# Optimization experiments

Hardware: AMD Instinct MI355X
Metric: run time of the kernel (lower is better)

Reference implementation:

```python
import jax, jax.numpy as jnp
import numpy as np

WS = 7          # window_size
HEADS = 6
HEAD_DIM = 32
DISP = WS // 2  # displacement = 3
NEG = -1e9      # stands in for -inf in shift masks (safe for grads/low precision)


def _rel_indices():
    # get_relative_distances(window_size) + window_size - 1
    pos = np.array([[i, j] for i in range(WS) for j in range(WS)])  # (49, 2)
    return pos[None, :, :] - pos[:, None, :] + WS - 1               # (49, 49, 2)


def _shift_mask(nw_h, nw_w):
    # per-window additive mask replicating upper_lower_mask / left_right_mask placement
    n = WS * WS
    ul = np.zeros((n, n), np.float32)
    ul[-DISP * WS:, :-DISP * WS] = NEG
    ul[:-DISP * WS, -DISP * WS:] = NEG
    m4 = np.zeros((WS, WS, WS, WS), np.float32)
    m4[:, -DISP:, :, :-DISP] = NEG
    m4[:, :-DISP, :, -DISP:] = NEG
    lr = m4.reshape(n, n)
    full = np.zeros((nw_h, nw_w, n, n), np.float32)
    full[-1, :] += ul              # dots[:, :, -nw_w:] += upper_lower_mask
    full[:, -1] += lr              # dots[:, :, nw_w-1::nw_w] += left_right_mask
    return full.reshape(nw_h * nw_w, n, n)


def setup_inputs() -> dict:
    key = jax.random.key(0)
    k1, k2, k3, k4 = jax.random.split(key, 4)
    dim, inner = 192, HEADS * HEAD_DIM
    return {
        "x": jax.random.normal(k1, (16, 56, 56, dim), jnp.float32),
        "w_qkv": jax.random.normal(k2, (dim, inner * 3), jnp.float32) * 0.02,
        "pos_embedding": jax.random.normal(k3, (2 * WS - 1, 2 * WS - 1), jnp.float32),
        "w_out": jax.random.normal(k4, (inner, dim), jnp.float32) * 0.02,
        "b_out": jnp.zeros((dim,), jnp.float32),
    }


def reference(x, w_qkv, pos_embedding, w_out, b_out):
    b, H, W, dim = x.shape
    nw_h, nw_w = H // WS, W // WS
    x = jnp.roll(x, (-DISP, -DISP), axis=(1, 2))          # shifted window
    qkv = x @ w_qkv                                       # [b,H,W,3*inner]
    q, k, v = jnp.split(qkv, 3, axis=-1)

    def to_windows(t):  # [b,H,W,inner] -> [b,h,nw,ws*ws,d]
        t = t.reshape(b, nw_h, WS, nw_w, WS, HEADS, HEAD_DIM)
        return t.transpose(0, 5, 1, 3, 2, 4, 6).reshape(b, HEADS, nw_h * nw_w, WS * WS, HEAD_DIM)

    q, k, v = to_windows(q), to_windows(k), to_windows(v)
    scale = HEAD_DIM ** -0.5
    dots = jnp.einsum('bhwid,bhwjd->bhwij', q, k) * scale  # [b,h,nw,49,49]

    rel = _rel_indices()
    bias = pos_embedding[rel[..., 0], rel[..., 1]]         # [49,49]
    dots = dots + bias
    dots = dots + jnp.asarray(_shift_mask(nw_h, nw_w))     # broadcast over b,h

    attn = jax.nn.softmax(dots, axis=-1)
    out = jnp.einsum('bhwij,bhwjd->bhwid', attn, v)        # [b,h,nw,49,d]
    out = out.reshape(b, HEADS, nw_h, nw_w, WS, WS, HEAD_DIM)
    out = out.transpose(0, 2, 4, 3, 5, 1, 6).reshape(b, H, W, HEADS * HEAD_DIM)
    out = out @ w_out + b_out
    return jnp.roll(out, (DISP, DISP), axis=(1, 2))
```

## Files before the change

### kernel.cpp

```cpp
#include <hip/hip_runtime.h>
#include <hip/hip_bf16.h>

typedef __bf16 bf16_t;
typedef __bf16 bf16x8 __attribute__((ext_vector_type(8)));
typedef float f32x4 __attribute__((ext_vector_type(4)));
typedef unsigned int u32;

#define NB 16
#define HW 56
#define DIM 192
#define N3 576
#define WS7 7
#define HEADS 6
#define HD 32
#define NTOK 49
#define MFMA(a, b, c) __builtin_amdgcn_mfma_f32_16x16x32_bf16(a, b, c, 0, 0, 0)

__device__ __forceinline__ void gld_lds16(const bf16_t* g, bf16_t* l) {
    __builtin_amdgcn_global_load_lds((const __attribute__((address_space(1))) u32*)g,
                                     (__attribute__((address_space(3))) u32*)l, 16, 0, 0);
}

__global__ __launch_bounds__(256) void prep_x_kernel(const float* __restrict__ x,
                                                     bf16_t* __restrict__ xb) {
    int idx = blockIdx.x * 256 + threadIdx.x;
    const int total = NB * HW * HW * (DIM / 8);
    if (idx >= total) return;
    int c8 = idx % (DIM / 8);
    int p  = idx / (DIM / 8);
    int xx = p % HW;
    int yy = (p / HW) % HW;
    int bb = p / (HW * HW);
    int ys = yy + 3; if (ys >= HW) ys -= HW;
    int xs = xx + 3; if (xs >= HW) xs -= HW;
    const float* src = x + ((size_t)(bb * HW + ys) * HW + xs) * DIM + c8 * 8;
    float4 a0 = *reinterpret_cast<const float4*>(src);
    float4 a1 = *reinterpret_cast<const float4*>(src + 4);
    bf16x8 o;
    o[0] = (bf16_t)a0.x; o[1] = (bf16_t)a0.y; o[2] = (bf16_t)a0.z; o[3] = (bf16_t)a0.w;
    o[4] = (bf16_t)a1.x; o[5] = (bf16_t)a1.y; o[6] = (bf16_t)a1.z; o[7] = (bf16_t)a1.w;
    *reinterpret_cast<bf16x8*>(xb + (size_t)idx * 8) = o;
}

__global__ __launch_bounds__(256) void prep_w_kernel(const float* __restrict__ wqkv,
                                                     const float* __restrict__ wout,
                                                     bf16_t* __restrict__ wqkvt,
                                                     bf16_t* __restrict__ woutt) {
    int idx = blockIdx.x * 256 + threadIdx.x;
    if (idx < N3 * DIM) {
        int k = idx % DIM, n = idx / DIM;
        wqkvt[idx] = (bf16_t)wqkv[(size_t)k * N3 + n];
    } else {
        int j = idx - N3 * DIM;
        if (j < DIM * DIM) {
            int k = j % DIM, n = j / DIM;
            woutt[j] = (bf16_t)wout[(size_t)k * DIM + n];
        }
    }
}

__global__ __launch_bounds__(256) void prep_tbl_kernel(const float* __restrict__ pe,
                                                       float* __restrict__ tbl) {
    int idx = blockIdx.x * 256 + threadIdx.x;
    if (idx >= 4 * 64 * 64) return;
    int v = idx >> 12, rem = idx & 4095, ti = rem >> 6, tj = rem & 63;
    float val = -1e9f;
    if (ti < NTOK && tj < NTOK) {
        int yi = ti / 7, xi = ti % 7, yj = tj / 7, xj = tj % 7;
        val = pe[(yj - yi + 6) * 13 + (xj - xi + 6)];
        bool mr = (v & 2) && ((yi >= 4) != (yj >= 4));
        bool mc = (v & 1) && ((xi >= 4) != (xj >= 4));
        if (mr || mc) val = -1e9f;
    }
    tbl[idx] = val;
}

__global__ __launch_bounds__(256) void qkv_gemm5(const bf16_t* __restrict__ xb,
                                                 const bf16_t* __restrict__ wt,
                                                 bf16_t* __restrict__ qkv) {
    __shared__ alignas(16) bf16_t bsh[64 * DIM];
    const int nblk = blockIdx.y;
    const int wave = threadIdx.x >> 6, lane = threadIdx.x & 63;
    const int lo = lane & 15, hi = lane >> 4;

    const bf16_t* bt = wt + (size_t)nblk * 64 * DIM;
#pragma unroll
    for (int i = 0; i < 6; i++) {
        int s = wave * 384 + i * 64 + lane;
        int g = s ^ ((s / 24) & 7);
        gld_lds16(bt + g * 8, bsh + (wave * 384 + i * 64) * 8);
    }

    const size_t rowbase = (size_t)blockIdx.x * 512 + wave * 32;
    const float qs = (nblk < 3) ? 0.17677669529663687f : 1.0f;

    auto load_tile = [&](bf16x8 (&a)[2][6], int t) {
        const bf16_t* ab = xb + (rowbase + t * 128 + lo) * DIM + hi * 8;
#pragma unroll
        for (int mtl = 0; mtl < 2; mtl++)
#pragma unroll
            for (int ks = 0; ks < 6; ks++)
                a[mtl][ks] = *reinterpret_cast<const bf16x8*>(ab + mtl * 16 * DIM + ks * 32);
    };

    auto compute_store = [&](bf16x8 (&a)[2][6], int t) {
        f32x4 acc[2][4];
#pragma unroll
        for (int mtl = 0; mtl < 2; mtl++)
#pragma unroll
            for (int ct = 0; ct < 4; ct++) acc[mtl][ct] = (f32x4){0.f, 0.f, 0.f, 0.f};
#pragma unroll
        for (int ks = 0; ks < 6; ks++)
#pragma unroll
            for (int ct = 0; ct < 4; ct++) {
                int r = ct * 16 + lo;
                int off = (ks * 64 + hi * 16) ^ ((r & 7) << 4);
                bf16x8 b = *reinterpret_cast<const bf16x8*>((const char*)bsh + r * 384 + off);
#pragma unroll
                for (int mtl = 0; mtl < 2; mtl++)
                    acc[mtl][ct] = MFMA(a[mtl][ks], b, acc[mtl][ct]);
            }
        const size_t rb = rowbase + t * 128;
#pragma unroll
        for (int mtl = 0; mtl < 2; mtl++)
#pragma unroll
            for (int ct = 0; ct < 4; ct++)
#pragma unroll
                for (int r = 0; r < 4; r++)
                    qkv[(rb + mtl * 16 + hi * 4 + r) * N3 + nblk * 64 + ct * 16 + lo] =
                        (bf16_t)(acc[mtl][ct][r] * qs);
    };

    bf16x8 A0[2][6], A1[2][6];
    load_tile(A0, 0);
    __syncthreads();

#pragma unroll
    for (int t = 0; t < 4; t += 2) {
        load_tile(A1, t + 1);
        compute_store(A0, t);
        if (t + 2 < 4) load_tile(A0, t + 2);
        compute_store(A1, t + 1);
    }
}

__global__ __launch_bounds__(256) void attn_kernel4(const bf16_t* __restrict__ qkv,
                                                    const float* __restrict__ tbl,
                                                    bf16_t* __restrict__ att) {
    const int win = blockIdx.x, h = blockIdx.y, bb = blockIdx.z;
    const int wh = win >> 3, ww = win & 7;
    const int mt = threadIdx.x >> 6;
    const int lane = threadIdx.x & 63;
    const int lo = lane & 15, hi = lane >> 4;

    __shared__ bf16_t P[64][72];
    __shared__ alignas(16) bf16_t VT[32][72];

    const int variant = ((wh == 7) ? 2 : 0) | ((ww == 7) ? 1 : 0);
    const float* tbase = tbl + ((size_t)variant << 12);

    auto tokoff = [&](int t) -> size_t {
        int ti = t / 7, tj = t % 7;
        return ((size_t)(bb * HW + wh * WS7 + ti) * HW + ww * WS7 + tj) * N3 + h * HD;
    };

    {
        const int t = mt * 16 + lo;
        bf16x8 v;
        if (t < NTOK) {
            v = *reinterpret_cast<const bf16x8*>(qkv + tokoff(t) + 2 * DIM + hi * 8);
        } else {
#pragma unroll
            for (int j = 0; j < 8; j++) v[j] = (bf16_t)0.f;
        }
#pragma unroll
        for (int j = 0; j < 8; j++) VT[hi * 8 + j][t] = v[j];
    }

    bf16x8 qf, kf[4];
    {
        int t = mt * 16 + lo;
        if (t < NTOK) {
            qf = *reinterpret_cast<const bf16x8*>(qkv + tokoff(t) + hi * 8);
        } else {
#pragma unroll
            for (int j = 0; j < 8; j++) qf[j] = (bf16_t)0.f;
        }
    }
#pragma unroll
    for (int ct = 0; ct < 4; ct++) {
        int t = ct * 16 + lo;
        if (t < NTOK) {
            kf[ct] = *reinterpret_cast<const bf16x8*>(qkv + tokoff(t) + DIM + hi * 8);
        } else {
#pragma unroll
            for (int j = 0; j < 8; j++) kf[ct][j] = (bf16_t)0.f;
        }
    }

    const f32x4 zero4 = {0.f, 0.f, 0.f, 0.f};
    f32x4 s[4];
#pragma unroll
    for (int ct = 0; ct < 4; ct++) s[ct] = MFMA(qf, kf[ct], zero4);

    float rinv[4];
#pragma unroll
    for (int r = 0; r < 4; r++) {
        int ti = mt * 16 + hi * 4 + r;
        const float* trow = tbase + ti * 64 + lo;
        float vals[4];
        float mx = -3e38f;
#pragma unroll
        for (int ct = 0; ct < 4; ct++) {
            float v = s[ct][r] + trow[ct * 16];
            vals[ct] = v;
            mx = fmaxf(mx, v);
        }
#pragma unroll
        for (int off = 1; off < 16; off <<= 1) mx = fmaxf(mx, __shfl_xor(mx, off));
        float sum = 0.f;
#pragma unroll
        for (int ct = 0; ct < 4; ct++) {
            float p = __expf(vals[ct] - mx);
            sum += p;
            P[ti][ct * 16 + lo] = (bf16_t)p;
        }
#pragma unroll
        for (int off = 1; off < 16; off <<= 1) sum += __shfl_xor(sum, off);
        rinv[r] = 1.f / sum;
    }

    __syncthreads();

    f32x4 o[2] = {zero4, zero4};
#pragma unroll
    for (int ks = 0; ks < 2; ks++) {
        bf16x8 pa = *reinterpret_cast<const bf16x8*>(&P[mt * 16 + lo][ks * 32 + hi * 8]);
#pragma unroll
        for (int c2 = 0; c2 < 2; c2++) {
            bf16x8 vb = *reinterpret_cast<const bf16x8*>(&VT[c2 * 16 + lo][ks * 32 + hi * 8]);
            o[c2] = MFMA(pa, vb, o[c2]);
        }
    }

#pragma unroll
    for (int r = 0; r < 4; r++) {
        int ti = mt * 16 + hi * 4 + r;
        if (ti < NTOK) {
            int y = wh * WS7 + ti / 7, xcol = ww * WS7 + ti % 7;
            size_t aoff = ((size_t)(bb * HW + y) * HW + xcol) * DIM + h * HD;
#pragma unroll
            for (int c2 = 0; c2 < 2; c2++)
                att[aoff + c2 * 16 + lo] = (bf16_t)(o[c2][r] * rinv[r]);
        }
    }
}

__global__ __launch_bounds__(256) void out_gemm2(const bf16_t* __restrict__ att,
                                                 const bf16_t* __restrict__ wt,
                                                 const float* __restrict__ bias,
                                                 float* __restrict__ out) {
    __shared__ alignas(16) bf16_t bsh[64 * DIM];
    const int mblk = blockIdx.x, nblk = blockIdx.y;
    const int wave = threadIdx.x >> 6, lane = threadIdx.x & 63;
    const int lo = lane & 15, hi = lane >> 4;

    const bf16_t* bt = wt + (size_t)nblk * 64 * DIM;
#pragma unroll
    for (int i = 0; i < 6; i++) {
        int s = wave * 384 + i * 64 + lane;
        int g = s ^ ((s / 24) & 7);
        gld_lds16(bt + g * 8, bsh + (wave * 384 + i * 64) * 8);
    }

    bf16x8 a[2][6];
    const bf16_t* ab = att + ((size_t)mblk * 128 + wave * 32 + lo) * DIM + hi * 8;
#pragma unroll
    for (int mt = 0; mt < 2; mt++)
#pragma unroll
        for (int ks = 0; ks < 6; ks++)
            a[mt][ks] = *reinterpret_cast<const bf16x8*>(ab + mt * 16 * DIM + ks * 32);

    f32x4 acc[2][4];
#pragma unroll
    for (int mt = 0; mt < 2; mt++)
#pragma unroll
        for (int ct = 0; ct < 4; ct++) acc[mt][ct] = (f32x4){0.f, 0.f, 0.f, 0.f};

    __syncthreads();

#pragma unroll
    for (int ks = 0; ks < 6; ks++)
#pragma unroll
        for (int ct = 0; ct < 4; ct++) {
            int r = ct * 16 + lo;
            int off = (ks * 64 + hi * 16) ^ ((r & 7) << 4);
            bf16x8 b = *reinterpret_cast<const bf16x8*>((const char*)bsh + r * 384 + off);
            acc[0][ct] = MFMA(a[0][ks], b, acc[0][ct]);
            acc[1][ct] = MFMA(a[1][ks], b, acc[1][ct]);
        }

    const int rb = mblk * 128 + wave * 32;
#pragma unroll
    for (int mt = 0; mt < 2; mt++)
#pragma unroll
        for (int r = 0; r < 4; r++) {
            int m = rb + mt * 16 + hi * 4 + r;
            int bb = m / (HW * HW);
            int rem = m - bb * HW * HW;
            int ya = rem / HW, xa = rem - ya * HW;
            int yo = ya + 3; if (yo >= HW) yo -= HW;
            int xo = xa + 3; if (xo >= HW) xo -= HW;
            size_t ob = ((size_t)(bb * HW + yo) * HW + xo) * DIM + nblk * 64;
#pragma unroll
            for (int ct = 0; ct < 4; ct++)
                out[ob + ct * 16 + lo] = acc[mt][ct][r] + bias[nblk * 64 + ct * 16 + lo];
        }
}

extern "C" void kernel_launch(void* const* d_in, const int* in_sizes, int n_in,
                              void* d_out, int out_size, void* d_ws, size_t ws_size,
                              hipStream_t stream) {
    const float* x    = (const float*)d_in[0];
    const float* wqkv = (const float*)d_in[1];
    const float* pe   = (const float*)d_in[2];
    const float* wout = (const float*)d_in[3];
    const float* bout = (const float*)d_in[4];
    float* out = (float*)d_out;

    char* ws = (char*)d_ws;
    const size_t XB_BYTES  = (size_t)NB * HW * HW * DIM * 2;
    const size_t QKV_BYTES = (size_t)NB * HW * HW * N3 * 2;
    const size_t ATT_BYTES = XB_BYTES;
    const size_t WQ_BYTES  = (size_t)N3 * DIM * 2;
    const size_t WO_BYTES  = (size_t)DIM * DIM * 2;
    bf16_t* xb    = (bf16_t*)ws;
    bf16_t* qkv   = (bf16_t*)(ws + XB_BYTES);
    bf16_t* att   = (bf16_t*)(ws + XB_BYTES + QKV_BYTES);
    bf16_t* wqkvt = (bf16_t*)(ws + XB_BYTES + QKV_BYTES + ATT_BYTES);
    bf16_t* woutt = (bf16_t*)(ws + XB_BYTES + QKV_BYTES + ATT_BYTES + WQ_BYTES);
    float*  tbl   = (float*)(ws + XB_BYTES + QKV_BYTES + ATT_BYTES + WQ_BYTES + WO_BYTES);

    prep_x_kernel<<<(NB * HW * HW * (DIM / 8) + 255) / 256, 256, 0, stream>>>(x, xb);
    prep_w_kernel<<<(N3 * DIM + DIM * DIM + 255) / 256, 256, 0, stream>>>(wqkv, wout, wqkvt, woutt);
    prep_tbl_kernel<<<64, 256, 0, stream>>>(pe, tbl);
    qkv_gemm5<<<dim3(98, 9), 256, 0, stream>>>(xb, wqkvt, qkv);
    attn_kernel4<<<dim3(64, HEADS, NB), 256, 0, stream>>>(qkv, tbl, att);
    out_gemm2<<<dim3(392, 3), 256, 0, stream>>>(att, woutt, bout, out);
}
```

Baseline: 176.7 us.

## Fuse QKV projection into window attention kernel, eliminating the qkv buffer

Removes the separate QKV GEMM. Each attention block now loads its window's 49 tokens of x, computes its own head's Q, K and V with MFMA against weights read straight from global memory, and stages them in LDS before the existing softmax and PV steps. This avoids writing and re-reading the large bf16 qkv intermediate. In exchange, x is re-read once per head, weight tiles are fetched through L2 by every block, and each block does more serial work. The grid is reordered so the six heads of a window run adjacently, improving L2 reuse of x.

New measurement: 232.2 us. +31.5%, slower.

```diff
diff --git a/kernel.cpp b/kernel.cpp
--- a/kernel.cpp
+++ b/kernel.cpp
@@ -75,134 +75,73 @@
     tbl[idx] = val;
 }
 
-__global__ __launch_bounds__(256) void qkv_gemm5(const bf16_t* __restrict__ xb,
-                                                 const bf16_t* __restrict__ wt,
-                                                 bf16_t* __restrict__ qkv) {
-    __shared__ alignas(16) bf16_t bsh[64 * DIM];
-    const int nblk = blockIdx.y;
-    const int wave = threadIdx.x >> 6, lane = threadIdx.x & 63;
-    const int lo = lane & 15, hi = lane >> 4;
-
-    const bf16_t* bt = wt + (size_t)nblk * 64 * DIM;
-#pragma unroll
-    for (int i = 0; i < 6; i++) {
-        int s = wave * 384 + i * 64 + lane;
-        int g = s ^ ((s / 24) & 7);
-        gld_lds16(bt + g * 8, bsh + (wave * 384 + i * 64) * 8);
-    }
-
-    const size_t rowbase = (size_t)blockIdx.x * 512 + wave * 32;
-    const float qs = (nblk < 3) ? 0.17677669529663687f : 1.0f;
-
-    auto load_tile = [&](bf16x8 (&a)[2][6], int t) {
-        const bf16_t* ab = xb + (rowbase + t * 128 + lo) * DIM + hi * 8;
-#pragma unroll
-        for (int mtl = 0; mtl < 2; mtl++)
-#pragma unroll
-            for (int ks = 0; ks < 6; ks++)
-                a[mtl][ks] = *reinterpret_cast<const bf16x8*>(ab + mtl * 16 * DIM + ks * 32);
-    };
-
-    auto compute_store = [&](bf16x8 (&a)[2][6], int t) {
-        f32x4 acc[2][4];
-#pragma unroll
-        for (int mtl = 0; mtl < 2; mtl++)
-#pragma unroll
-            for (int ct = 0; ct < 4; ct++) acc[mtl][ct] = (f32x4){0.f, 0.f, 0.f, 0.f};
-#pragma unroll
-        for (int ks = 0; ks < 6; ks++)
-#pragma unroll
-            for (int ct = 0; ct < 4; ct++) {
-                int r = ct * 16 + lo;
-                int off = (ks * 64 + hi * 16) ^ ((r & 7) << 4);
-                bf16x8 b = *reinterpret_cast<const bf16x8*>((const char*)bsh + r * 384 + off);
-#pragma unroll
-                for (int mtl = 0; mtl < 2; mtl++)
-                    acc[mtl][ct] = MFMA(a[mtl][ks], b, acc[mtl][ct]);
-            }
-        const size_t rb = rowbase + t * 128;
-#pragma unroll
-        for (int mtl = 0; mtl < 2; mtl++)
-#pragma unroll
-            for (int ct = 0; ct < 4; ct++)
-#pragma unroll
-                for (int r = 0; r < 4; r++)
-                    qkv[(rb + mtl * 16 + hi * 4 + r) * N3 + nblk * 64 + ct * 16 + lo] =
-                        (bf16_t)(acc[mtl][ct][r] * qs);
-    };
-
-    bf16x8 A0[2][6], A1[2][6];
-    load_tile(A0, 0);
-    __syncthreads();
-
-#pragma unroll
-    for (int t = 0; t < 4; t += 2) {
-        load_tile(A1, t + 1);
-        compute_store(A0, t);
-        if (t + 2 < 4) load_tile(A0, t + 2);
-        compute_store(A1, t + 1);
-    }
-}
-
-__global__ __launch_bounds__(256) void attn_kernel4(const bf16_t* __restrict__ qkv,
-                                                    const float* __restrict__ tbl,
-                                                    bf16_t* __restrict__ att) {
-    const int win = blockIdx.x, h = blockIdx.y, bb = blockIdx.z;
+__global__ __launch_bounds__(256, 4) void fused_attn_kernel(const bf16_t* __restrict__ xb,
+                                                            const bf16_t* __restrict__ wt,
+                                                            const float* __restrict__ tbl,
+                                                            bf16_t* __restrict__ att) {
+    const int h = blockIdx.x, win = blockIdx.y, bb = blockIdx.z;
     const int wh = win >> 3, ww = win & 7;
     const int mt = threadIdx.x >> 6;
     const int lane = threadIdx.x & 63;
     const int lo = lane & 15, hi = lane >> 4;
 
-    __shared__ bf16_t P[64][72];
-    __shared__ alignas(16) bf16_t VT[32][72];
+    __shared__ alignas(16) bf16_t Qs[64 * 40];
+    __shared__ alignas(16) bf16_t Ks[64 * 40];
+    __shared__ alignas(16) bf16_t VTs[32 * 72];
+    __shared__ alignas(16) bf16_t P[64 * 72];
+
+    bf16x8 a[6];
+    {
+        int t = mt * 16 + lo;
+        if (t >= NTOK) t = 0;
+        int y = wh * WS7 + t / 7, xcol = ww * WS7 + t % 7;
+        const bf16_t* ar = xb + ((size_t)(bb * HW + y) * HW + xcol) * DIM + hi * 8;
+#pragma unroll
+        for (int ks = 0; ks < 6; ks++)
+            a[ks] = *reinterpret_cast<const bf16x8*>(ar + ks * 32);
+    }
+
+    f32x4 acc6[3][2];
+#pragma unroll
+    for (int s = 0; s < 3; s++)
+#pragma unroll
+        for (int nt = 0; nt < 2; nt++) acc6[s][nt] = (f32x4){0.f, 0.f, 0.f, 0.f};
+
+#pragma unroll
+    for (int s = 0; s < 3; s++)
+#pragma unroll
+        for (int nt = 0; nt < 2; nt++) {
+            const bf16_t* bp = wt + (size_t)(s * DIM + h * HD + nt * 16 + lo) * DIM + hi * 8;
+#pragma unroll
+            for (int ks = 0; ks < 6; ks++) {
+                bf16x8 bf = *reinterpret_cast<const bf16x8*>(bp + ks * 32);
+                acc6[s][nt] = MFMA(a[ks], bf, acc6[s][nt]);
+            }
+        }
+
+    const float qs = 0.17677669529663687f;
+#pragma unroll
+    for (int nt = 0; nt < 2; nt++)
+#pragma unroll
+        for (int r = 0; r < 4; r++) {
+            int tok = mt * 16 + hi * 4 + r;
+            Qs[tok * 40 + nt * 16 + lo] = (bf16_t)(acc6[0][nt][r] * qs);
+            Ks[tok * 40 + nt * 16 + lo] = (bf16_t)acc6[1][nt][r];
+            VTs[(nt * 16 + lo) * 72 + tok] = (bf16_t)acc6[2][nt][r];
+        }
+    __syncthreads();
+
+    const f32x4 zero4 = {0.f, 0.f, 0.f, 0.f};
+    bf16x8 qa = *reinterpret_cast<const bf16x8*>(&Qs[(mt * 16 + lo) * 40 + hi * 8]);
+    f32x4 s4[4];
+#pragma unroll
+    for (int ct = 0; ct < 4; ct++) {
+        bf16x8 kb = *reinterpret_cast<const bf16x8*>(&Ks[(ct * 16 + lo) * 40 + hi * 8]);
+        s4[ct] = MFMA(qa, kb, zero4);
+    }
 
     const int variant = ((wh == 7) ? 2 : 0) | ((ww == 7) ? 1 : 0);
     const float* tbase = tbl + ((size_t)variant << 12);
-
-    auto tokoff = [&](int t) -> size_t {
-        int ti = t / 7, tj = t % 7;
-        return ((size_t)(bb * HW + wh * WS7 + ti) * HW + ww * WS7 + tj) * N3 + h * HD;
-    };
-
-    {
-        const int t = mt * 16 + lo;
-        bf16x8 v;
-        if (t < NTOK) {
-            v = *reinterpret_cast<const bf16x8*>(qkv + tokoff(t) + 2 * DIM + hi * 8);
-        } else {
-#pragma unroll
-            for (int j = 0; j < 8; j++) v[j] = (bf16_t)0.f;
-        }
-#pragma unroll
-        for (int j = 0; j < 8; j++) VT[hi * 8 + j][t] = v[j];
-    }
-
-    bf16x8 qf, kf[4];
-    {
-        int t = mt * 16 + lo;
-        if (t < NTOK) {
-            qf = *reinterpret_cast<const bf16x8*>(qkv + tokoff(t) + hi * 8);
-        } else {
-#pragma unroll
-            for (int j = 0; j < 8; j++) qf[j] = (bf16_t)0.f;
-        }
-    }
-#pragma unroll
-    for (int ct = 0; ct < 4; ct++) {
-        int t = ct * 16 + lo;
-        if (t < NTOK) {
-            kf[ct] = *reinterpret_cast<const bf16x8*>(qkv + tokoff(t) + DIM + hi * 8);
-        } else {
-#pragma unroll
-            for (int j = 0; j < 8; j++) kf[ct][j] = (bf16_t)0.f;
-        }
-    }
-
-    const f32x4 zero4 = {0.f, 0.f, 0.f, 0.f};
-    f32x4 s[4];
-#pragma unroll
-    for (int ct = 0; ct < 4; ct++) s[ct] = MFMA(qf, kf[ct], zero4);
-
     float rinv[4];
 #pragma unroll
     for (int r = 0; r < 4; r++) {
@@ -212,7 +151,7 @@
         float mx = -3e38f;
 #pragma unroll
         for (int ct = 0; ct < 4; ct++) {
-            float v = s[ct][r] + trow[ct * 16];
+            float v = s4[ct][r] + trow[ct * 16];
             vals[ct] = v;
             mx = fmaxf(mx, v);
         }
@@ -223,22 +162,20 @@
         for (int ct = 0; ct < 4; ct++) {
             float p = __expf(vals[ct] - mx);
             sum += p;
-            P[ti][ct * 16 + lo] = (bf16_t)p;
+            P[ti * 72 + ct * 16 + lo] = (bf16_t)p;
         }
 #pragma unroll
         for (int off = 1; off < 16; off <<= 1) sum += __shfl_xor(sum, off);
         rinv[r] = 1.f / sum;
     }
 
-    __syncthreads();
-
     f32x4 o[2] = {zero4, zero4};
 #pragma unroll
     for (int ks = 0; ks < 2; ks++) {
-        bf16x8 pa = *reinterpret_cast<const bf16x8*>(&P[mt * 16 + lo][ks * 32 + hi * 8]);
+        bf16x8 pa = *reinterpret_cast<const bf16x8*>(&P[(mt * 16 + lo) * 72 + ks * 32 + hi * 8]);
 #pragma unroll
         for (int c2 = 0; c2 < 2; c2++) {
-            bf16x8 vb = *reinterpret_cast<const bf16x8*>(&VT[c2 * 16 + lo][ks * 32 + hi * 8]);
+            bf16x8 vb = *reinterpret_cast<const bf16x8*>(&VTs[(c2 * 16 + lo) * 72 + ks * 32 + hi * 8]);
             o[c2] = MFMA(pa, vb, o[c2]);
         }
     }
@@ -330,21 +267,18 @@
 
     char* ws = (char*)d_ws;
     const size_t XB_BYTES  = (size_t)NB * HW * HW * DIM * 2;
-    const size_t QKV_BYTES = (size_t)NB * HW * HW * N3 * 2;
     const size_t ATT_BYTES = XB_BYTES;
     const size_t WQ_BYTES  = (size_t)N3 * DIM * 2;
     const size_t WO_BYTES  = (size_t)DIM * DIM * 2;
     bf16_t* xb    = (bf16_t*)ws;
-    bf16_t* qkv   = (bf16_t*)(ws + XB_BYTES);
-    bf16_t* att   = (bf16_t*)(ws + XB_BYTES + QKV_BYTES);
-    bf16_t* wqkvt = (bf16_t*)(ws + XB_BYTES + QKV_BYTES + ATT_BYTES);
-    bf16_t* woutt = (bf16_t*)(ws + XB_BYTES + QKV_BYTES + ATT_BYTES + WQ_BYTES);
-    float*  tbl   = (float*)(ws + XB_BYTES + QKV_BYTES + ATT_BYTES + WQ_BYTES + WO_BYTES);
+    bf16_t* att   = (bf16_t*)(ws + XB_BYTES);
+    bf16_t* wqkvt = (bf16_t*)(ws + XB_BYTES + ATT_BYTES);
+    bf16_t* woutt = (bf16_t*)(ws + XB_BYTES + ATT_BYTES + WQ_BYTES);
+    float*  tbl   = (float*)(ws + XB_BYTES + ATT_BYTES + WQ_BYTES + WO_BYTES);
 
     prep_x_kernel<<<(NB * HW * HW * (DIM / 8) + 255) / 256, 256, 0, stream>>>(x, xb);
     prep_w_kernel<<<(N3 * DIM + DIM * DIM + 255) / 256, 256, 0, stream>>>(wqkv, wout, wqkvt, woutt);
     prep_tbl_kernel<<<64, 256, 0, stream>>>(pe, tbl);
-    qkv_gemm5<<<dim3(98, 9), 256, 0, stream>>>(xb, wqkvt, qkv);
-    attn_kernel4<<<dim3(64, HEADS, NB), 256, 0, stream>>>(qkv, tbl, att);
+    fused_attn_kernel<<<dim3(HEADS, 64, NB), 256, 0, stream>>>(xb, wqkvt, tbl, att);
     out_gemm2<<<dim3(392, 3), 256, 0, stream>>>(att, woutt, bout, out);
 }
```
